# Kernel tuning notes

Hardware: AMD Instinct MI355X
Metric: run time of the kernel (lower is better)

Reference implementation:

```python
import jax, jax.numpy as jnp
import numpy as np

N = 50000
E = 1600000
IN_DIM = 16
HID = 64
HEADS = 2


def _gat_layer(x, src, dst, W, a_src, a_dst, b, heads, ch, n):
    # PyG GATConv with add_self_loops=True, negative_slope=0.2, concat heads.
    h = (x @ W).reshape(n, heads, ch)                       # [N,H,C]
    loop = jnp.arange(n)
    s = jnp.concatenate([src, loop])                        # self loops appended
    d = jnp.concatenate([dst, loop])
    alpha_s = (h * a_src).sum(-1)                           # [N,H]
    alpha_d = (h * a_dst).sum(-1)
    e = jax.nn.leaky_relu(alpha_s[s] + alpha_d[d], 0.2)     # [E+N,H]
    m = jax.ops.segment_max(e, d, num_segments=n)           # softmax over incoming edges
    ee = jnp.exp(e - m[d])
    denom = jax.ops.segment_sum(ee, d, num_segments=n)
    alpha = ee / denom[d]
    out = jax.ops.segment_sum(h[s] * alpha[:, :, None], d, num_segments=n)
    return out.reshape(n, heads * ch) + b


def setup_inputs() -> dict:
    key = jax.random.key(0)
    ks = jax.random.split(key, 20)
    gn = lambda k, sh, sc: (jax.random.normal(k, sh, dtype=jnp.float32) * sc)
    x = gn(ks[0], (N, IN_DIM), 1.0)
    edge_index = jax.random.randint(ks[1], (2, E), 0, N, dtype=jnp.int64)
    inp = {
        'x': x, 'edge_index': edge_index,
        'W1': gn(ks[2], (IN_DIM, HEADS * HID), 0.2),
        'as1': gn(ks[3], (HEADS, HID), 0.2), 'ad1': gn(ks[4], (HEADS, HID), 0.2),
        'b1': gn(ks[5], (HEADS * HID,), 0.05),
        'W2': gn(ks[6], (HEADS * HID, HID), 0.1),
        'as2': gn(ks[7], (1, HID), 0.2), 'ad2': gn(ks[8], (1, HID), 0.2),
        'b2': gn(ks[9], (HID,), 0.05),
        'mW1': gn(ks[10], (2 * HID, HID), 0.1), 'mb1': gn(ks[11], (HID,), 0.05),
        'mW2': gn(ks[12], (HID, HID), 0.1), 'mb2': gn(ks[13], (HID,), 0.05),
        'mW3': gn(ks[14], (HID, HID), 0.1), 'mb3': gn(ks[15], (HID,), 0.05),
        'mW4': gn(ks[16], (HID, 1), 0.1), 'mb4': gn(ks[17], (1,), 0.05),
    }
    return inp


def reference(x, edge_index, W1, as1, ad1, b1, W2, as2, ad2, b2,
              mW1, mb1, mW2, mb2, mW3, mb3, mW4, mb4):
    row, col = edge_index[0], edge_index[1]
    n = x.shape[0]
    h = jax.nn.relu(_gat_layer(x, row, col, W1, as1, ad1, b1, HEADS, HID, n))
    h = jax.nn.relu(_gat_layer(h, row, col, W2, as2, ad2, b2, 1, HID, n))
    ef = jnp.concatenate([h[row], h[col]], axis=1)          # [E, 2*HID]
    z = jax.nn.relu(ef @ mW1 + mb1)
    z = jax.nn.relu(z @ mW2 + mb2)
    z = jax.nn.relu(z @ mW3 + mb3)
    return (z @ mW4 + mb4).squeeze(-1)                      # [E]
```

## Files before the change

kernel.cpp:

```cpp
#include <hip/hip_runtime.h>
#include <hip/hip_bf16.h>
#include <hip/hip_fp16.h>
#include <math.h>

#define N_NODES 50000
#define N_EDGES 1600000
#define IN_DIM 16
#define HID 64
#define NBLK 6250
#define NB1 49
#define SM_SHIFT 20.0f

typedef __attribute__((ext_vector_type(8))) _Float16 half8v;
typedef __attribute__((ext_vector_type(16))) float f32x16;

union H8 { uint4 u4; half8v v; };

__device__ __forceinline__ float lrelu(float v) { return v > 0.f ? v : 0.2f * v; }

__device__ __forceinline__ float wave_reduce_sum(float v) {
    #pragma unroll
    for (int off = 32; off > 0; off >>= 1) v += __shfl_down(v, off, 64);
    return v;
}

__global__ void k_prep(const float* __restrict__ W1, const float* __restrict__ as1,
                       const float* __restrict__ ad1, float* __restrict__ qs, float* __restrict__ qd,
                       const float* __restrict__ mW2, const float* __restrict__ mW3,
                       __half* __restrict__ W2th, __half* __restrict__ W3th) {
    int t = threadIdx.x;
    if (blockIdx.x == 64) {
        if (t < 32) {
            int i = t >> 1, h = t & 1;
            float s = 0.f, d = 0.f;
            for (int c = 0; c < 64; c++) {
                float w = W1[i * 128 + h * 64 + c];
                s = fmaf(w, as1[h * 64 + c], s);
                d = fmaf(w, ad1[h * 64 + c], d);
            }
            qs[i * 2 + h] = s; qd[i * 2 + h] = d;
        }
    } else {
        int b = blockIdx.x;
        W2th[b * 64 + t] = __float2half(mW2[t * 64 + b]);
        W3th[b * 64 + t] = __float2half(mW3[t * 64 + b]);
    }
}

__global__ void k1n(const float* __restrict__ x, const float* __restrict__ qs,
                    const float* __restrict__ qd, float* __restrict__ al_s, float* __restrict__ al_d) {
    int n = blockIdx.x * 256 + threadIdx.x;
    if (n >= N_NODES) return;
    float s0 = 0.f, s1 = 0.f, d0 = 0.f, d1 = 0.f;
    #pragma unroll
    for (int i = 0; i < IN_DIM; i++) {
        float xv = x[n * IN_DIM + i];
        s0 = fmaf(xv, qs[i * 2 + 0], s0);
        s1 = fmaf(xv, qs[i * 2 + 1], s1);
        d0 = fmaf(xv, qd[i * 2 + 0], d0);
        d1 = fmaf(xv, qd[i * 2 + 1], d1);
    }
    al_s[n * 2 + 0] = s0; al_s[n * 2 + 1] = s1;
    al_d[n * 2 + 0] = d0; al_d[n * 2 + 1] = d1;
}

#define SCAN_B 256
__global__ void k_scan2(int* __restrict__ bsum, int nblocks) {
    __shared__ int sh[SCAN_B];
    int v = (threadIdx.x < nblocks) ? bsum[threadIdx.x] : 0;
    sh[threadIdx.x] = v;
    __syncthreads();
    for (int o = 1; o < SCAN_B; o <<= 1) {
        int t = (threadIdx.x >= o) ? sh[threadIdx.x - o] : 0;
        __syncthreads();
        sh[threadIdx.x] += t;
        __syncthreads();
    }
    if (threadIdx.x < nblocks) bsum[threadIdx.x] = sh[threadIdx.x] - v;
}

__global__ void g_scan1(const int* __restrict__ in, int* __restrict__ out,
                        int* __restrict__ bsum, int n) {
    __shared__ int sh[SCAN_B];
    int gid = blockIdx.x * SCAN_B + threadIdx.x;
    int v = (gid < n) ? in[gid] : 0;
    sh[threadIdx.x] = v;
    __syncthreads();
    for (int o = 1; o < SCAN_B; o <<= 1) {
        int t = (threadIdx.x >= o) ? sh[threadIdx.x - o] : 0;
        __syncthreads();
        sh[threadIdx.x] += t;
        __syncthreads();
    }
    int incl = sh[threadIdx.x];
    if (gid < n) out[gid] = incl - v;
    if (threadIdx.x == SCAN_B - 1) bsum[blockIdx.x] = incl;
}
__global__ void g_add(int* __restrict__ out, const int* __restrict__ bsum, int n) {
    int gid = blockIdx.x * SCAN_B + threadIdx.x;
    if (gid < n) out[gid] += bsum[blockIdx.x];
}

__global__ __launch_bounds__(256) void s_hist1(const int* __restrict__ dst,
                                               int* __restrict__ cnt1) {
    __shared__ int c[NB1];
    if (threadIdx.x < NB1) c[threadIdx.x] = 0;
    __syncthreads();
    int e = blockIdx.x * 256 + threadIdx.x;
    atomicAdd(&c[dst[e] >> 10], 1);
    __syncthreads();
    if (threadIdx.x < NB1) cnt1[threadIdx.x * NBLK + blockIdx.x] = c[threadIdx.x];
}

__global__ __launch_bounds__(256) void s_scatter1(const int* __restrict__ src,
                                                  const int* __restrict__ dst,
                                                  const int* __restrict__ basep1,
                                                  unsigned long long* __restrict__ tmp) {
    __shared__ int c[NB1], base[NB1];
    if (threadIdx.x < NB1) c[threadIdx.x] = 0;
    __syncthreads();
    int e = blockIdx.x * 256 + threadIdx.x;
    int d = dst[e], s = src[e];
    int k = d >> 10;
    int rank = atomicAdd(&c[k], 1);
    __syncthreads();
    if (threadIdx.x < NB1) base[threadIdx.x] = basep1[threadIdx.x * NBLK + blockIdx.x];
    __syncthreads();
    unsigned long long v = ((unsigned long long)e << 32) |
                           (((unsigned)d << 16) | (unsigned)s);
    tmp[base[k] + rank] = v;
}

__global__ __launch_bounds__(1024) void k_sort2b(const unsigned long long* __restrict__ tmp,
                                                 const int* __restrict__ basep1,
                                                 int* __restrict__ offp,
                                                 unsigned* __restrict__ ssd,
                                                 int* __restrict__ eid) {
    __shared__ int cnt[1024];
    int b = blockIdx.x, t = threadIdx.x;
    int d0 = b << 10;
    int nd = N_NODES - d0; if (nd > 1024) nd = 1024;
    cnt[t] = 0;
    __syncthreads();
    int ebeg = basep1[b * NBLK];
    int eend = (b == NB1 - 1) ? N_EDGES : basep1[(b + 1) * NBLK];
    for (int i = ebeg + t; i < eend; i += 1024) {
        unsigned lo = (unsigned)tmp[i];
        atomicAdd(&cnt[(lo >> 16) - d0], 1);
    }
    __syncthreads();
    int v = cnt[t];
    for (int o = 1; o < 1024; o <<= 1) {
        int tv = (t >= o) ? cnt[t - o] : 0;
        __syncthreads();
        cnt[t] += tv;
        __syncthreads();
    }
    int cur = ebeg + cnt[t] - v;
    if (t < nd) offp[d0 + t] = cur;
    if (b == NB1 - 1 && t == 0) offp[N_NODES] = N_EDGES;
    __syncthreads();
    cnt[t] = cur;
    __syncthreads();
    for (int i = ebeg + t; i < eend; i += 1024) {
        unsigned long long v64 = tmp[i];
        unsigned lo = (unsigned)v64;
        int pos = atomicAdd(&cnt[(lo >> 16) - d0], 1);
        ssd[pos] = lo;
        eid[pos] = (int)(v64 >> 32);
    }
}

__global__ void k3n(const float* __restrict__ x, const float* __restrict__ als,
                    const float* __restrict__ ald,
                    const int* __restrict__ off, const unsigned* __restrict__ ssd,
                    float* __restrict__ accx, float* __restrict__ denb) {
    int wid = threadIdx.x >> 6, lane = threadIdx.x & 63;
    int half = lane >> 5, sub = lane & 31, head = sub >> 4, ch = sub & 15;
    int d = blockIdx.x * 8 + wid * 2 + half;
    if (d >= N_NODES) return;
    int beg = off[d], end = off[d + 1];
    float adv = ald[d * 2 + head];
    float es = lrelu(als[d * 2 + head] + adv);
    float ws = __expf(es - SM_SHIFT);
    float den0 = ws, den1 = 0.f;
    float a0 = ws * x[d * IN_DIM + ch], a1 = 0.f;
    const int srcb = (lane & 32) + (head << 4);
    for (int c = beg; c < end; c += 16) {
        int nchunk = end - c; if (nchunk > 16) nchunk = 16;
        float wexp = 0.f;
        if ((sub & 15) < nchunk) {
            int s = (int)(ssd[c + (sub & 15)] & 0xffffu);
            wexp = __expf(lrelu(als[s * 2 + head] + adv) - SM_SHIFT);
        }
        if (nchunk == 16) {
            int sv[16];
            #pragma unroll
            for (int t = 0; t < 16; t++) sv[t] = (int)(ssd[c + t] & 0xffffu);
            #pragma unroll
            for (int t = 0; t < 16; t++) {
                float wv = __shfl(wexp, srcb + t, 64);
                float xv = x[sv[t] * IN_DIM + ch];
                if (t & 1) { den1 += wv; a1 = fmaf(wv, xv, a1); }
                else       { den0 += wv; a0 = fmaf(wv, xv, a0); }
            }
        } else {
            for (int t = 0; t < nchunk; t++) {
                float wv = __shfl(wexp, srcb + t, 64);
                int s = (int)(ssd[c + t] & 0xffffu);
                den0 += wv; a0 = fmaf(wv, x[s * IN_DIM + ch], a0);
            }
        }
    }
    accx[d * 32 + sub] = a0 + a1;
    if ((sub & 15) == 0) denb[d * 2 + head] = den0 + den1;
}

__global__ __launch_bounds__(256) void k4n(
    const float* __restrict__ accx, const float* __restrict__ denb,
    const float* __restrict__ W1, const float* __restrict__ b1,
    const float* __restrict__ W2, const float* __restrict__ as2, const float* __restrict__ ad2,
    __half* __restrict__ h2h, float* __restrict__ al_s, float* __restrict__ al_d) {
    __shared__ float W1s[16 * 128];
    __shared__ float W2s[128 * 64];
    __shared__ float st[4][160];
    for (int t = threadIdx.x; t < 16 * 128; t += 256) W1s[t] = W1[t];
    for (int t = threadIdx.x; t < 128 * 64; t += 256) W2s[t] = W2[t];
    __syncthreads();
    int wid = threadIdx.x >> 6, lane = threadIdx.x & 63;
    for (int n = blockIdx.x * 4 + wid; n < N_NODES; n += gridDim.x * 4) {
        if (lane < 32) st[wid][lane] = accx[n * 32 + lane];
        float den0 = denb[n * 2], den1 = denb[n * 2 + 1];
        float ta = 0.f, tb = 0.f;
        #pragma unroll
        for (int i = 0; i < 16; i++) {
            ta = fmaf(st[wid][i],      W1s[i * 128 + lane],      ta);
            tb = fmaf(st[wid][16 + i], W1s[i * 128 + 64 + lane], tb);
        }
        ta = fmaxf(ta / den0 + b1[lane], 0.f);
        tb = fmaxf(tb / den1 + b1[64 + lane], 0.f);
        st[wid][32 + lane] = ta;
        st[wid][96 + lane] = tb;
        float acc = 0.f;
        #pragma unroll 8
        for (int k = 0; k < 128; k++) acc = fmaf(st[wid][32 + k], W2s[k * 64 + lane], acc);
        h2h[n * 64 + lane] = __float2half(acc);
        float ps = wave_reduce_sum(acc * as2[lane]);
        float pd = wave_reduce_sum(acc * ad2[lane]);
        if (lane == 0) { al_s[n] = ps; al_d[n] = pd; }
    }
}

__global__ __launch_bounds__(64) void k5a(
    const __half* __restrict__ h2h, const float* __restrict__ als, const float* __restrict__ ald,
    const float* __restrict__ b2, const int* __restrict__ off, const unsigned* __restrict__ ssd,
    float* __restrict__ out2) {
    __shared__ float wbuf[64];
    int d = blockIdx.x;
    int lane = threadIdx.x;
    int beg = off[d], end = off[d + 1];
    float adv = ald[d];
    float es = lrelu(als[d] + adv);
    float ws = __expf(es - SM_SHIFT);
    float den0 = ws, den1 = 0.f;
    float a0 = ws * __half2float(h2h[d * 64 + lane]), a1 = 0.f;
    for (int c = beg; c < end; c += 64) {
        int idx = c + lane;
        if (idx < end) {
            int s = (int)(ssd[idx] & 0xffffu);
            wbuf[lane] = __expf(lrelu(als[s] + adv) - SM_SHIFT);
        }
        int nchunk = end - c; if (nchunk > 64) nchunk = 64;
        int t = 0;
        for (; t + 7 < nchunk; t += 8) {
            int sv[8]; float wv[8], vv[8];
            #pragma unroll
            for (int q = 0; q < 8; q++) sv[q] = (int)(ssd[c + t + q] & 0xffffu);
            #pragma unroll
            for (int q = 0; q < 8; q++) wv[q] = wbuf[t + q];
            #pragma unroll
            for (int q = 0; q < 8; q++) vv[q] = __half2float(h2h[sv[q] * 64 + lane]);
            den0 += wv[0]; a0 = fmaf(wv[0], vv[0], a0);
            den1 += wv[1]; a1 = fmaf(wv[1], vv[1], a1);
            den0 += wv[2]; a0 = fmaf(wv[2], vv[2], a0);
            den1 += wv[3]; a1 = fmaf(wv[3], vv[3], a1);
            den0 += wv[4]; a0 = fmaf(wv[4], vv[4], a0);
            den1 += wv[5]; a1 = fmaf(wv[5], vv[5], a1);
            den0 += wv[6]; a0 = fmaf(wv[6], vv[6], a0);
            den1 += wv[7]; a1 = fmaf(wv[7], vv[7], a1);
        }
        for (; t < nchunk; t++) {
            int s = (int)(ssd[c + t] & 0xffffu);
            float wv = wbuf[t];
            den0 += wv; a0 = fmaf(wv, __half2float(h2h[s * 64 + lane]), a0);
        }
    }
    out2[d * 64 + lane] = fmaxf((a0 + a1) / (den0 + den1) + b2[lane], 0.f);
}

__global__ __launch_bounds__(256) void k5b(const float* __restrict__ out2,
                                           const float* __restrict__ mW1,
                                           const float* __restrict__ mb1,
                                           __half* __restrict__ Uh, __half* __restrict__ Vh) {
    __shared__ float Ws[128 * 64];
    __shared__ float o2s[4][64];
    for (int t = threadIdx.x; t < 128 * 64; t += 256) Ws[t] = mW1[t];
    __syncthreads();
    int wid = threadIdx.x >> 6, lane = threadIdx.x & 63;
    for (int n = blockIdx.x * 4 + wid; n < N_NODES; n += gridDim.x * 4) {
        o2s[wid][lane] = out2[n * 64 + lane];
        float au = mb1[lane], av = 0.f;
        #pragma unroll 8
        for (int k = 0; k < 64; k++) {
            float ov = o2s[wid][k];
            au = fmaf(ov, Ws[k * 64 + lane], au);
            av = fmaf(ov, Ws[(64 + k) * 64 + lane], av);
        }
        Uh[n * 64 + lane] = __float2half(au);
        Vh[n * 64 + lane] = __float2half(av);
    }
}

__global__ __launch_bounds__(512) void k7h(
    const unsigned* __restrict__ ssd, const int* __restrict__ eid,
    const __half* __restrict__ Uh, const __half* __restrict__ Vh,
    const __half* __restrict__ W2th, const __half* __restrict__ W3th,
    const float* __restrict__ mb2, const float* __restrict__ mb3,
    const float* __restrict__ mW4, const float* __restrict__ mb4,
    float* __restrict__ out)
{
    __shared__ unsigned short Wf[2][4096];
    __shared__ float mbS[3][64];
    const int t = threadIdx.x;
    {
        int mA = t >> 8, kb = (t >> 6) & 3, l = t & 63;
        int src = (mA * 32 + (l & 31)) * 64 + kb * 16 + (l >> 5) * 8;
        *(uint4*)&Wf[0][t * 8] = *(const uint4*)(W2th + src);
        *(uint4*)&Wf[1][t * 8] = *(const uint4*)(W3th + src);
        if (t < 64) mbS[0][t] = mb2[t];
        else if (t < 128) mbS[1][t - 64] = mb3[t - 64];
        else if (t < 192) mbS[2][t - 128] = mW4[t - 128];
    }
    __syncthreads();

    const int nb = gridDim.x, q8 = nb >> 3, r8 = nb & 7;
    const int xcd = blockIdx.x & 7, bidx = blockIdx.x >> 3;
    const int wg = (xcd < r8) ? xcd * (q8 + 1) + bidx
                              : r8 * (q8 + 1) + (xcd - r8) * q8 + bidx;

    const int wid = t >> 6, lane = t & 63;
    const int tbase = wg * 256 + wid * 32;
    const int l31 = lane & 31;
    const int h = lane >> 5;
    const int ksub = h * 8;

    unsigned sd = ssd[tbase + l31];
    int rA = (int)(sd & 0xffffu);
    int cA = (int)(sd >> 16);
    const __half* urow = Uh + (size_t)rA * 64 + ksub;
    const __half* vrow = Vh + (size_t)cA * 64 + ksub;

    f32x16 c2[2];
    #pragma unroll
    for (int mA = 0; mA < 2; mA++)
        #pragma unroll
        for (int q = 0; q < 4; q++) {
            float4 b = *(const float4*)&mbS[0][mA * 32 + 4 * h + q * 8];
            c2[mA][q * 4 + 0] = b.x; c2[mA][q * 4 + 1] = b.y;
            c2[mA][q * 4 + 2] = b.z; c2[mA][q * 4 + 3] = b.w;
        }

    #pragma unroll
    for (int kb = 0; kb < 4; kb++) {
        H8 uvu, vvu, zz;
        uvu.u4 = *(const uint4*)(urow + kb * 16);
        vvu.u4 = *(const uint4*)(vrow + kb * 16);
        {
            half8v s = uvu.v + vvu.v;
            #pragma unroll
            for (int j = 0; j < 8; j++) {
                _Float16 a = s[j];
                zz.v[j] = a > (_Float16)0 ? a : (_Float16)0;
            }
        }
        #pragma unroll
        for (int mA = 0; mA < 2; mA++) {
            const int f = (mA * 4 + kb) * 64 + lane;
            half8v ah = *(const half8v*)&Wf[0][f * 8];
            c2[mA] = __builtin_amdgcn_mfma_f32_32x32x16_f16(ah, zz.v, c2[mA], 0, 0, 0);
        }
    }

    half8v B3[4];
    #pragma unroll
    for (int kbp = 0; kbp < 4; kbp++) {
        const int mAs = kbp >> 1, kbl = kbp & 1;
        half8v t8;
        #pragma unroll
        for (int b = 0; b < 4; b++) {
            float u = fmaxf(c2[mAs][8 * kbl + b], 0.f);
            float v = fmaxf(c2[mAs][8 * kbl + 4 + b], 0.f);
            float su = __shfl_xor(u, 32, 64);
            float sv = __shfl_xor(v, 32, 64);
            t8[b]     = (_Float16)(h ? sv : u);
            t8[4 + b] = (_Float16)(h ? v : su);
        }
        B3[kbp] = t8;
    }

    f32x16 c3[2];
    #pragma unroll
    for (int mA = 0; mA < 2; mA++)
        #pragma unroll
        for (int q = 0; q < 4; q++) {
            float4 b = *(const float4*)&mbS[1][mA * 32 + 4 * h + q * 8];
            c3[mA][q * 4 + 0] = b.x; c3[mA][q * 4 + 1] = b.y;
            c3[mA][q * 4 + 2] = b.z; c3[mA][q * 4 + 3] = b.w;
        }

    #pragma unroll
    for (int kbp = 0; kbp < 4; kbp++) {
        #pragma unroll
        for (int mA = 0; mA < 2; mA++) {
            const int f = (mA * 4 + kbp) * 64 + lane;
            half8v ah = *(const half8v*)&Wf[1][f * 8];
            c3[mA] = __builtin_amdgcn_mfma_f32_32x32x16_f16(ah, B3[kbp], c3[mA], 0, 0, 0);
        }
    }

    float p = 0.f;
    #pragma unroll
    for (int mA = 0; mA < 2; mA++)
        #pragma unroll
        for (int q = 0; q < 4; q++) {
            float4 w4 = *(const float4*)&mbS[2][mA * 32 + 4 * h + q * 8];
            p = fmaf(fmaxf(c3[mA][q * 4 + 0], 0.f), w4.x, p);
            p = fmaf(fmaxf(c3[mA][q * 4 + 1], 0.f), w4.y, p);
            p = fmaf(fmaxf(c3[mA][q * 4 + 2], 0.f), w4.z, p);
            p = fmaf(fmaxf(c3[mA][q * 4 + 3], 0.f), w4.w, p);
        }
    p += __shfl_xor(p, 32, 64);
    int eA = eid[tbase + l31];
    if (lane < 32) out[eA] = p + mb4[0];
}

extern "C" void kernel_launch(void* const* d_in, const int* in_sizes, int n_in,
                              void* d_out, int out_size, void* d_ws, size_t ws_size,
                              hipStream_t stream) {
    const float* x   = (const float*)d_in[0];
    const int*   ei  = (const int*)d_in[1];
    const float* W1  = (const float*)d_in[2];
    const float* as1 = (const float*)d_in[3];
    const float* ad1 = (const float*)d_in[4];
    const float* b1  = (const float*)d_in[5];
    const float* W2  = (const float*)d_in[6];
    const float* as2 = (const float*)d_in[7];
    const float* ad2 = (const float*)d_in[8];
    const float* b2  = (const float*)d_in[9];
    const float* mW1 = (const float*)d_in[10];
    const float* mb1 = (const float*)d_in[11];
    const float* mW2 = (const float*)d_in[12];
    const float* mb2 = (const float*)d_in[13];
    const float* mW3 = (const float*)d_in[14];
    const float* mb3 = (const float*)d_in[15];
    const float* mW4 = (const float*)d_in[16];
    const float* mb4 = (const float*)d_in[17];
    float* out = (float*)d_out;
    const int* row = ei;
    const int* col = ei + N_EDGES;

    char* w = (char*)d_ws;
    __half*   Uh    = (__half*)w;
    __half*   Vh    = (__half*)(w + 6400000);
    float*    out2  = (float*)(w + 12800000);
    __half*   h2h   = (__half*)(w + 25600000);
    unsigned* ssd   = (unsigned*)(w + 32000000);
    int*      eid   = (int*)(w + 38400000);
    unsigned long long* tmp = (unsigned long long*)(w + 44800000);
    int*      offp  = (int*)(w + 57800000);
    float*    al_s2 = (float*)(w + 58200064);
    float*    al_d2 = (float*)(w + 58400064);
    int*      bsum  = (int*)(w + 58600064);
    float*    qs    = (float*)(w + 58605056);
    float*    qd    = (float*)(w + 58605184);
    __half*   W2th  = (__half*)(w + 58605312);
    __half*   W3th  = W2th + 4096;
    int*      cnt1  = (int*)(w + 58988992);
    int*      basep1= (int*)(w + 60214000);
    int*      bsumA = (int*)(w + 61439008);
    float*    accx  = (float*)(w + 12800000);
    float*    denb  = (float*)(w + 19200000);
    float*    al_s1 = (float*)(w + 19600000);
    float*    al_d1 = (float*)(w + 20000000);

    k_prep<<<65, 64, 0, stream>>>(W1, as1, ad1, qs, qd, mW2, mW3, W2th, W3th);
    k1n<<<(N_NODES + 255) / 256, 256, 0, stream>>>(x, qs, qd, al_s1, al_d1);
    s_hist1<<<NBLK, 256, 0, stream>>>(col, cnt1);
    {
        int n1 = NB1 * NBLK;
        int nb1 = (n1 + SCAN_B - 1) / SCAN_B;
        int nb2 = (nb1 + SCAN_B - 1) / SCAN_B;
        g_scan1<<<nb1, SCAN_B, 0, stream>>>(cnt1, basep1, bsumA, n1);
        g_scan1<<<nb2, SCAN_B, 0, stream>>>(bsumA, bsumA, bsum, nb1);
        k_scan2<<<1, SCAN_B, 0, stream>>>(bsum, nb2);
        g_add<<<nb2, SCAN_B, 0, stream>>>(bsumA, bsum, nb1);
        g_add<<<nb1, SCAN_B, 0, stream>>>(basep1, bsumA, n1);
    }
    s_scatter1<<<NBLK, 256, 0, stream>>>(row, col, basep1, tmp);
    k_sort2b<<<NB1, 1024, 0, stream>>>(tmp, basep1, offp, ssd, eid);
    k3n<<<N_NODES / 8, 256, 0, stream>>>(x, al_s1, al_d1, offp, ssd, accx, denb);
    k4n<<<768, 256, 0, stream>>>(accx, denb, W1, b1, W2, as2, ad2, h2h, al_s2, al_d2);
    k5a<<<N_NODES, 64, 0, stream>>>(h2h, al_s2, al_d2, b2, offp, ssd, out2);
    k5b<<<1024, 256, 0, stream>>>(out2, mW1, mb1, Uh, Vh);
    k7h<<<NBLK, 512, 0, stream>>>(ssd, eid, Uh, Vh,
                                  W2th, W3th,
                                  mb2, mb3, mW4, mb4, out);
}
```

Before: 326.5 us.

## Run edge MLP in original edge order and drop edge-id tracking from sort

After: 307.2 us. 5.9% less time.

```diff
diff --git a/kernel.cpp b/kernel.cpp
--- a/kernel.cpp
+++ b/kernel.cpp
@@ -115,7 +115,7 @@
 __global__ __launch_bounds__(256) void s_scatter1(const int* __restrict__ src,
                                                   const int* __restrict__ dst,
                                                   const int* __restrict__ basep1,
-                                                  unsigned long long* __restrict__ tmp) {
+                                                  unsigned* __restrict__ tmp) {
     __shared__ int c[NB1], base[NB1];
     if (threadIdx.x < NB1) c[threadIdx.x] = 0;
     __syncthreads();
@@ -126,16 +126,13 @@
     __syncthreads();
     if (threadIdx.x < NB1) base[threadIdx.x] = basep1[threadIdx.x * NBLK + blockIdx.x];
     __syncthreads();
-    unsigned long long v = ((unsigned long long)e << 32) |
-                           (((unsigned)d << 16) | (unsigned)s);
-    tmp[base[k] + rank] = v;
-}
-
-__global__ __launch_bounds__(1024) void k_sort2b(const unsigned long long* __restrict__ tmp,
+    tmp[base[k] + rank] = ((unsigned)d << 16) | (unsigned)s;
+}
+
+__global__ __launch_bounds__(1024) void k_sort2b(const unsigned* __restrict__ tmp,
                                                  const int* __restrict__ basep1,
                                                  int* __restrict__ offp,
-                                                 unsigned* __restrict__ ssd,
-                                                 int* __restrict__ eid) {
+                                                 unsigned* __restrict__ ssd) {
     __shared__ int cnt[1024];
     int b = blockIdx.x, t = threadIdx.x;
     int d0 = b << 10;
@@ -145,8 +142,7 @@
     int ebeg = basep1[b * NBLK];
     int eend = (b == NB1 - 1) ? N_EDGES : basep1[(b + 1) * NBLK];
     for (int i = ebeg + t; i < eend; i += 1024) {
-        unsigned lo = (unsigned)tmp[i];
-        atomicAdd(&cnt[(lo >> 16) - d0], 1);
+        atomicAdd(&cnt[(tmp[i] >> 16) - d0], 1);
     }
     __syncthreads();
     int v = cnt[t];
@@ -163,11 +159,9 @@
     cnt[t] = cur;
     __syncthreads();
     for (int i = ebeg + t; i < eend; i += 1024) {
-        unsigned long long v64 = tmp[i];
-        unsigned lo = (unsigned)v64;
+        unsigned lo = tmp[i];
         int pos = atomicAdd(&cnt[(lo >> 16) - d0], 1);
         ssd[pos] = lo;
-        eid[pos] = (int)(v64 >> 32);
     }
 }
 
@@ -321,8 +315,8 @@
     }
 }
 
-__global__ __launch_bounds__(512) void k7h(
-    const unsigned* __restrict__ ssd, const int* __restrict__ eid,
+__global__ __launch_bounds__(512) void k7j(
+    const int* __restrict__ row, const int* __restrict__ col,
     const __half* __restrict__ Uh, const __half* __restrict__ Vh,
     const __half* __restrict__ W2th, const __half* __restrict__ W3th,
     const float* __restrict__ mb2, const float* __restrict__ mb3,
@@ -343,20 +337,14 @@
     }
     __syncthreads();
 
-    const int nb = gridDim.x, q8 = nb >> 3, r8 = nb & 7;
-    const int xcd = blockIdx.x & 7, bidx = blockIdx.x >> 3;
-    const int wg = (xcd < r8) ? xcd * (q8 + 1) + bidx
-                              : r8 * (q8 + 1) + (xcd - r8) * q8 + bidx;
-
     const int wid = t >> 6, lane = t & 63;
-    const int tbase = wg * 256 + wid * 32;
+    const int tbase = blockIdx.x * 256 + wid * 32;
     const int l31 = lane & 31;
     const int h = lane >> 5;
     const int ksub = h * 8;
 
-    unsigned sd = ssd[tbase + l31];
-    int rA = (int)(sd & 0xffffu);
-    int cA = (int)(sd >> 16);
+    int rA = row[tbase + l31];
+    int cA = col[tbase + l31];
     const __half* urow = Uh + (size_t)rA * 64 + ksub;
     const __half* vrow = Vh + (size_t)cA * 64 + ksub;
 
@@ -440,8 +428,7 @@
             p = fmaf(fmaxf(c3[mA][q * 4 + 3], 0.f), w4.w, p);
         }
     p += __shfl_xor(p, 32, 64);
-    int eA = eid[tbase + l31];
-    if (lane < 32) out[eA] = p + mb4[0];
+    if (lane < 32) out[tbase + l31] = p + mb4[0];
 }
 
 extern "C" void kernel_launch(void* const* d_in, const int* in_sizes, int n_in,
@@ -475,8 +462,7 @@
     float*    out2  = (float*)(w + 12800000);
     __half*   h2h   = (__half*)(w + 25600000);
     unsigned* ssd   = (unsigned*)(w + 32000000);
-    int*      eid   = (int*)(w + 38400000);
-    unsigned long long* tmp = (unsigned long long*)(w + 44800000);
+    unsigned* tmp   = (unsigned*)(w + 38400000);
     int*      offp  = (int*)(w + 57800000);
     float*    al_s2 = (float*)(w + 58200064);
     float*    al_d2 = (float*)(w + 58400064);
@@ -507,12 +493,12 @@
         g_add<<<nb1, SCAN_B, 0, stream>>>(basep1, bsumA, n1);
     }
     s_scatter1<<<NBLK, 256, 0, stream>>>(row, col, basep1, tmp);
-    k_sort2b<<<NB1, 1024, 0, stream>>>(tmp, basep1, offp, ssd, eid);
+    k_sort2b<<<NB1, 1024, 0, stream>>>(tmp, basep1, offp, ssd);
     k3n<<<N_NODES / 8, 256, 0, stream>>>(x, al_s1, al_d1, offp, ssd, accx, denb);
     k4n<<<768, 256, 0, stream>>>(accx, denb, W1, b1, W2, as2, ad2, h2h, al_s2, al_d2);
     k5a<<<N_NODES, 64, 0, stream>>>(h2h, al_s2, al_d2, b2, offp, ssd, out2);
     k5b<<<1024, 256, 0, stream>>>(out2, mW1, mb1, Uh, Vh);
-    k7h<<<NBLK, 512, 0, stream>>>(ssd, eid, Uh, Vh,
+    k7j<<<NBLK, 512, 0, stream>>>(row, col, Uh, Vh,
                                   W2th, W3th,
                                   mb2, mb3, mW4, mb4, out);
 }
```
